# Kernel tuning notes

Hardware: AMD Instinct MI355X
Metric: run time of the kernel (lower is better)

The kernel has to match this reference:

```python
import jax, jax.numpy as jnp
import numpy as np

B = 16384      # batch
H = 512        # experts_hidden
E = 5          # num_experts
T = 2          # num_tasks
OUT = 128      # fixed protein expert output width (from .view(-1, E, 1, 128))


def setup_inputs() -> dict:
    key = jax.random.key(0)
    ks = jax.random.split(key, 12)
    s = 0.02  # init scale
    return {
        "share_x": jax.random.normal(ks[0], (B, H), jnp.float32),
        "task_x0": jax.random.normal(ks[1], (B, H), jnp.float32),
        "task_x1": jax.random.normal(ks[2], (B, H), jnp.float32),
        # shared experts: stacked weights for all E experts
        "share_W1": jax.random.normal(ks[3], (E, H, H), jnp.float32) * s,
        "share_b1": jnp.zeros((E, H), jnp.float32),
        "share_W2": jax.random.normal(ks[4], (E, H, OUT), jnp.float32) * s,
        "share_b2": jnp.zeros((E, OUT), jnp.float32),
        # task experts: [T, E, ...]
        "task_W1": jax.random.normal(ks[5], (T, E, H, H), jnp.float32) * s,
        "task_b1": jnp.zeros((T, E, H), jnp.float32),
        "task_W2": jax.random.normal(ks[6], (T, E, H, OUT), jnp.float32) * s,
        "task_b2": jnp.zeros((T, E, OUT), jnp.float32),
    }


def _expert_bank(x, W1, b1, W2, b2):
    """Run all E experts on x in one batched GEMM pair.

    x: [B, H]; W1: [E, H, H]; W2: [E, H, OUT].
    Equivalent to torch.concat([e(x) for e in experts], dim=0)
    followed by .view(-1, E, 1, OUT).
    """
    h = jax.nn.relu(jnp.einsum('bh,ehk->ebk', x, W1) + b1[:, None, :])  # [E,B,H]
    o = jnp.einsum('ebk,eko->ebo', h, W2) + b2[:, None, :]              # [E,B,OUT]
    # concat along dim 0 == flatten (E,B) -> E*B, then view(-1, E, 1, OUT)
    return o.reshape(-1, E, 1, OUT)


def reference(share_x, task_x0, task_x1,
              share_W1, share_b1, share_W2, share_b2,
              task_W1, task_b1, task_W2, task_b2):
    share_out = _expert_bank(share_x, share_W1, share_b1, share_W2, share_b2)
    task_xs = (task_x0, task_x1)
    task_outs = tuple(
        _expert_bank(task_xs[i], task_W1[i], task_b1[i], task_W2[i], task_b2[i])
        for i in range(T)
    )
    return (share_out,) + task_outs
```

## Files before the change

kernel.cpp:

```cpp
#include <hip/hip_runtime.h>

#define H 512
#define OW 128
#define NB 16384

typedef float f32x4 __attribute__((ext_vector_type(4)));
typedef short short8 __attribute__((ext_vector_type(8)));
typedef unsigned short ushort8v __attribute__((ext_vector_type(8)));

static __device__ __forceinline__ unsigned short f2bf(float f) {
    union { float f; unsigned u; } v; v.f = f;
    return (unsigned short)((v.u + 0x7FFFu + ((v.u >> 16) & 1u)) >> 16);
}

static __device__ __forceinline__ f32x4 mfma16(short8 a, short8 b, f32x4 c) {
    return __builtin_amdgcn_mfma_f32_16x16x32_bf16(a, b, c, 0, 0, 0);
}

static __device__ __forceinline__ void gll16(const unsigned short* g, unsigned short* l) {
    __builtin_amdgcn_global_load_lds(
        (__attribute__((address_space(1))) void*)g,
        (__attribute__((address_space(3))) void*)l, 16, 0, 0);
}

static __device__ __forceinline__ short8 sw_read(const unsigned short* l, int row, int ch) {
    return *(const short8*)&l[row * 64 + ((ch ^ (row & 7)) << 3)];
}

__global__ void prep_w1(const float* __restrict__ share_W1,
                        const float* __restrict__ task_W1,
                        unsigned short* __restrict__ w1t) {
    const int inst = blockIdx.z;
    const float* src = (inst < 5) ? (share_W1 + (size_t)inst * H * H)
                                  : (task_W1 + (size_t)(inst - 5) * H * H);
    unsigned short* dst = w1t + (size_t)inst * H * H;
    const int g = blockIdx.x * 256 + threadIdx.x;
    const int n = g & (H - 1);
    const int kc = g >> 9;
    float v[8];
#pragma unroll
    for (int i = 0; i < 8; ++i) v[i] = src[(size_t)(kc * 8 + i) * H + n];
    ushort8v o;
#pragma unroll
    for (int i = 0; i < 8; ++i) o[i] = f2bf(v[i]);
    *(ushort8v*)&dst[(size_t)n * H + kc * 8] = o;
}

__global__ void prep_w2(const float* __restrict__ share_W2,
                        const float* __restrict__ task_W2,
                        unsigned short* __restrict__ w2t) {
    const int inst = blockIdx.z;
    const float* src = (inst < 5) ? (share_W2 + (size_t)inst * H * OW)
                                  : (task_W2 + (size_t)(inst - 5) * H * OW);
    unsigned short* dst = w2t + (size_t)inst * OW * H;
    const int g = blockIdx.x * 256 + threadIdx.x;
    const int n = g & (OW - 1);
    const int kc = g >> 7;
    float v[8];
#pragma unroll
    for (int i = 0; i < 8; ++i) v[i] = src[(size_t)(kc * 8 + i) * OW + n];
    ushort8v o;
#pragma unroll
    for (int i = 0; i < 8; ++i) o[i] = f2bf(v[i]);
    *(ushort8v*)&dst[(size_t)n * H + kc * 8] = o;
}

__global__ void prep_x(const float* __restrict__ x0, const float* __restrict__ x1,
                       const float* __restrict__ x2, unsigned short* __restrict__ xb) {
    const int z = blockIdx.z;
    const float* s = (z == 0) ? x0 : (z == 1 ? x1 : x2);
    const size_t g = (size_t)(blockIdx.x * 256 + threadIdx.x) * 8;
    float4 a = *(const float4*)&s[g];
    float4 b = *(const float4*)&s[g + 4];
    ushort8v o;
    o[0] = f2bf(a.x); o[1] = f2bf(a.y); o[2] = f2bf(a.z); o[3] = f2bf(a.w);
    o[4] = f2bf(b.x); o[5] = f2bf(b.y); o[6] = f2bf(b.z); o[7] = f2bf(b.w);
    *(ushort8v*)&xb[(size_t)z * NB * H + g] = o;
}

__global__ __launch_bounds__(256, 2) void fused(
    const unsigned short* __restrict__ xb, const unsigned short* __restrict__ w1t,
    const unsigned short* __restrict__ w2t,
    const float* __restrict__ share_b1, const float* __restrict__ task_b1,
    const float* __restrict__ share_b2, const float* __restrict__ task_b2,
    float* __restrict__ out)
{
    __shared__ unsigned short smem[33792];
    unsigned short* sA  = smem;
    unsigned short* sB  = smem + 8192;
    unsigned short* sH  = smem + 16384;
    unsigned short* sW0 = smem;
    unsigned short* sW1 = smem + 8192;

    const int tid = threadIdx.x;
    const int lane = tid & 63;
    const int wave = tid >> 6;
    const int wy = wave >> 1, wx = wave & 1;
    const int lm = lane & 15, lq = lane >> 4;
    const int prow = lane >> 3;
    const int lch  = (lane & 7) ^ prow;

    const int swz = (blockIdx.x & 7) * 240 + (blockIdx.x >> 3);
    const int z = swz / 640;
    const int rzi = swz % 640;
    const int rowtile = rzi / 5;
    const int e = rzi % 5;
    const int inst = z * 5 + e;

    const unsigned short* xp  = xb + ((size_t)z * NB + rowtile * 128) * H;
    const unsigned short* w1p = w1t + (size_t)inst * H * H;
    const unsigned short* w2p = w2t + (size_t)inst * OW * H;
    const float* b1 = (z == 0) ? (share_b1 + e * H) : (task_b1 + ((z - 1) * 5 + e) * H);
    const float* b2 = (z == 0) ? (share_b2 + e * OW) : (task_b2 + ((z - 1) * 5 + e) * OW);
    float* op = out + ((size_t)inst * NB + rowtile * 128) * OW;

    const f32x4 zero4 = {0.f, 0.f, 0.f, 0.f};
    f32x4 acc2[4][4];
#pragma unroll
    for (int i = 0; i < 4; ++i)
#pragma unroll
        for (int j = 0; j < 4; ++j) acc2[i][j] = zero4;

    for (int nt = 0; nt < 4; ++nt) {
        const unsigned short* wnp = w1p + (size_t)(nt * 128) * H;

        f32x4 acc1[4][4];
#pragma unroll
        for (int i = 0; i < 4; ++i)
#pragma unroll
            for (int j = 0; j < 4; ++j) acc1[i][j] = zero4;

        for (int kt = 0; kt < 8; ++kt) {
            __syncthreads();
#pragma unroll
            for (int t = 0; t < 4; ++t) {
                const int row = wave * 32 + t * 8 + prow;
                const int lo = wave * 2048 + t * 512;
                gll16(&xp [(size_t)row * H + kt * 64 + lch * 8], &sA[lo]);
                gll16(&wnp[(size_t)row * H + kt * 64 + lch * 8], &sB[lo]);
            }
            __syncthreads();
#pragma unroll
            for (int kk = 0; kk < 2; ++kk) {
                short8 af[4], bfr[4];
#pragma unroll
                for (int i = 0; i < 4; ++i) af[i] = sw_read(sA, wy * 64 + i * 16 + lm, kk * 4 + lq);
#pragma unroll
                for (int j = 0; j < 4; ++j) bfr[j] = sw_read(sB, wx * 64 + j * 16 + lm, kk * 4 + lq);
#pragma unroll
                for (int i = 0; i < 4; ++i)
#pragma unroll
                    for (int j = 0; j < 4; ++j) acc1[i][j] = mfma16(af[i], bfr[j], acc1[i][j]);
            }
        }
        __syncthreads();

#pragma unroll
        for (int t = 0; t < 4; ++t) {
            const int row = wave * 32 + t * 8 + prow;
            const int lo = wave * 2048 + t * 512;
            gll16(&w2p[(size_t)row * H + nt * 128 +      lch * 8], &sW0[lo]);
            gll16(&w2p[(size_t)row * H + nt * 128 + 64 + lch * 8], &sW1[lo]);
        }

#pragma unroll
        for (int j = 0; j < 4; ++j) {
            const int col = wx * 64 + j * 16 + lm;
            const float b1v = b1[nt * 128 + col];
#pragma unroll
            for (int i = 0; i < 4; ++i)
#pragma unroll
                for (int rr = 0; rr < 4; ++rr) {
                    const int row = wy * 64 + i * 16 + lq * 4 + rr;
                    sH[row * 136 + col] = f2bf(fmaxf(acc1[i][j][rr] + b1v, 0.f));
                }
        }
        __syncthreads();

#pragma unroll
        for (int kk = 0; kk < 4; ++kk) {
            short8 af[4], bfr[4];
#pragma unroll
            for (int i = 0; i < 4; ++i)
                af[i] = *(const short8*)&sH[(wy * 64 + i * 16 + lm) * 136 + kk * 32 + lq * 8];
#pragma unroll
            for (int j = 0; j < 4; ++j)
                bfr[j] = sw_read((kk & 2) ? sW1 : sW0, wx * 64 + j * 16 + lm, (kk & 1) * 4 + lq);
#pragma unroll
            for (int i = 0; i < 4; ++i)
#pragma unroll
                for (int j = 0; j < 4; ++j) acc2[i][j] = mfma16(af[i], bfr[j], acc2[i][j]);
        }
    }

#pragma unroll
    for (int j = 0; j < 4; ++j) {
        const int col = wx * 64 + j * 16 + lm;
        const float b2v = b2[col];
#pragma unroll
        for (int i = 0; i < 4; ++i)
#pragma unroll
            for (int rr = 0; rr < 4; ++rr) {
                const int row = wy * 64 + i * 16 + lq * 4 + rr;
                op[(size_t)row * OW + col] = acc2[i][j][rr] + b2v;
            }
    }
}

extern "C" void kernel_launch(void* const* d_in, const int* in_sizes, int n_in,
                              void* d_out, int out_size, void* d_ws, size_t ws_size,
                              hipStream_t stream) {
    const float* share_x  = (const float*)d_in[0];
    const float* task_x0  = (const float*)d_in[1];
    const float* task_x1  = (const float*)d_in[2];
    const float* share_W1 = (const float*)d_in[3];
    const float* share_b1 = (const float*)d_in[4];
    const float* share_W2 = (const float*)d_in[5];
    const float* share_b2 = (const float*)d_in[6];
    const float* task_W1  = (const float*)d_in[7];
    const float* task_b1  = (const float*)d_in[8];
    const float* task_W2  = (const float*)d_in[9];
    const float* task_b2  = (const float*)d_in[10];
    float* out = (float*)d_out;

    unsigned short* w1t = (unsigned short*)d_ws;
    unsigned short* w2t = w1t + (size_t)15 * H * H;
    unsigned short* xb  = w2t + (size_t)15 * OW * H;

    prep_w1<<<dim3(128, 1, 15), 256, 0, stream>>>(share_W1, task_W1, w1t);
    prep_w2<<<dim3(32, 1, 15), 256, 0, stream>>>(share_W2, task_W2, w2t);
    prep_x <<<dim3(4096, 1, 3), 256, 0, stream>>>(share_x, task_x0, task_x1, xb);
    fused<<<1920, 256, 0, stream>>>(xb, w1t, w2t, share_b1, task_b1,
                                    share_b2, task_b2, out);
}
```

Before: 414.4 us.

## Double-buffer GEMM1 K-loop with async LDS loads and register-resident W2 fragments

Restructures the first GEMM's K loop into a double-buffered pipeline with 32-wide K steps. The next stage's global-to-LDS loads are issued while the current stage computes, using explicit vmcnt waits and raw s_barrier instead of full __syncthreads. W2 is pre-permuted on the host-side prep kernel into MFMA fragment order, so each wave loads its B fragments straight into registers rather than staging them through LDS. MFMA sections are also wrapped in s_setprio. This adds register pressure (16 short8 for W2), relies on hand-counted vmcnt values being correct, and the next tile's first stages are prefetched across the nt boundary.

```diff
diff --git a/kernel.cpp b/kernel.cpp
--- a/kernel.cpp
+++ b/kernel.cpp
@@ -23,9 +23,9 @@
         (__attribute__((address_space(3))) void*)l, 16, 0, 0);
 }
 
-static __device__ __forceinline__ short8 sw_read(const unsigned short* l, int row, int ch) {
-    return *(const short8*)&l[row * 64 + ((ch ^ (row & 7)) << 3)];
-}
+#define WAITB(n) asm volatile("s_waitcnt vmcnt(" #n ")\n\ts_barrier" ::: "memory")
+#define RELB()   asm volatile("s_barrier" ::: "memory")
+#define CFENCE() asm volatile("" ::: "memory")
 
 __global__ void prep_w1(const float* __restrict__ share_W1,
                         const float* __restrict__ task_W1,
@@ -48,21 +48,26 @@
 
 __global__ void prep_w2(const float* __restrict__ share_W2,
                         const float* __restrict__ task_W2,
-                        unsigned short* __restrict__ w2t) {
+                        unsigned short* __restrict__ w2f) {
     const int inst = blockIdx.z;
     const float* src = (inst < 5) ? (share_W2 + (size_t)inst * H * OW)
                                   : (task_W2 + (size_t)(inst - 5) * H * OW);
-    unsigned short* dst = w2t + (size_t)inst * OW * H;
+    unsigned short* dst = w2f + (size_t)inst * H * OW;
     const int g = blockIdx.x * 256 + threadIdx.x;
-    const int n = g & (OW - 1);
-    const int kc = g >> 7;
+    const int l  = g & 63;
+    const int f  = (g >> 6) & 15;
+    const int kk = f >> 2, j = f & 3;
+    const int wx = (g >> 10) & 1;
+    const int nt = (g >> 11) & 3;
+    const int n  = wx * 64 + j * 16 + (l & 15);
+    const int k0 = nt * 128 + kk * 32 + ((l >> 4) & 3) * 8;
     float v[8];
 #pragma unroll
-    for (int i = 0; i < 8; ++i) v[i] = src[(size_t)(kc * 8 + i) * OW + n];
+    for (int i = 0; i < 8; ++i) v[i] = src[(size_t)(k0 + i) * OW + n];
     ushort8v o;
 #pragma unroll
     for (int i = 0; i < 8; ++i) o[i] = f2bf(v[i]);
-    *(ushort8v*)&dst[(size_t)n * H + kc * 8] = o;
+    *(ushort8v*)&dst[(size_t)g * 8] = o;
 }
 
 __global__ void prep_x(const float* __restrict__ x0, const float* __restrict__ x1,
@@ -80,25 +85,22 @@
 
 __global__ __launch_bounds__(256, 2) void fused(
     const unsigned short* __restrict__ xb, const unsigned short* __restrict__ w1t,
-    const unsigned short* __restrict__ w2t,
+    const unsigned short* __restrict__ w2f,
     const float* __restrict__ share_b1, const float* __restrict__ task_b1,
     const float* __restrict__ share_b2, const float* __restrict__ task_b2,
     float* __restrict__ out)
 {
     __shared__ unsigned short smem[33792];
-    unsigned short* sA  = smem;
-    unsigned short* sB  = smem + 8192;
-    unsigned short* sH  = smem + 16384;
-    unsigned short* sW0 = smem;
-    unsigned short* sW1 = smem + 8192;
+    unsigned short* sH = smem + 16384;
 
     const int tid = threadIdx.x;
     const int lane = tid & 63;
     const int wave = tid >> 6;
     const int wy = wave >> 1, wx = wave & 1;
     const int lm = lane & 15, lq = lane >> 4;
-    const int prow = lane >> 3;
-    const int lch  = (lane & 7) ^ prow;
+    const int r4 = lane >> 2;
+    const int c4 = lane & 3;
+    const int sc4 = c4 ^ (r4 & 3);
 
     const int swz = (blockIdx.x & 7) * 240 + (blockIdx.x >> 3);
     const int z = swz / 640;
@@ -109,7 +111,7 @@
 
     const unsigned short* xp  = xb + ((size_t)z * NB + rowtile * 128) * H;
     const unsigned short* w1p = w1t + (size_t)inst * H * H;
-    const unsigned short* w2p = w2t + (size_t)inst * OW * H;
+    const unsigned short* w2b = w2f + (size_t)inst * H * OW + (size_t)lane * 8;
     const float* b1 = (z == 0) ? (share_b1 + e * H) : (task_b1 + ((z - 1) * 5 + e) * H);
     const float* b2 = (z == 0) ? (share_b2 + e * OW) : (task_b2 + ((z - 1) * 5 + e) * OW);
     float* op = out + ((size_t)inst * NB + rowtile * 128) * OW;
@@ -121,47 +123,67 @@
 #pragma unroll
         for (int j = 0; j < 4; ++j) acc2[i][j] = zero4;
 
+    f32x4 acc1[4][4];
+
+    auto STAGE = [&](int kt, int buf, const unsigned short* wsrc) {
+        unsigned short* a = smem + buf * 4096;
+        unsigned short* b = smem + 8192 + buf * 4096;
+        const int ko = kt * 32 + sc4 * 8;
+#pragma unroll
+        for (int t = 0; t < 2; ++t) {
+            gll16(&xp  [(size_t)(wave * 32 + t * 16 + r4) * H + ko], &a[wave * 1024 + t * 512]);
+            gll16(&wsrc[(size_t)(wave * 32 + t * 16 + r4) * H + ko], &b[wave * 1024 + t * 512]);
+        }
+    };
+
+    auto COMPUTE = [&](int buf) {
+        const unsigned short* a = smem + buf * 4096;
+        const unsigned short* b = smem + 8192 + buf * 4096;
+        const int sw = (lq ^ (lm & 3)) << 3;
+        short8 af[4], bq[4];
+#pragma unroll
+        for (int i = 0; i < 4; ++i) af[i] = *(const short8*)&a[(wy * 64 + i * 16 + lm) * 32 + sw];
+#pragma unroll
+        for (int j = 0; j < 4; ++j) bq[j] = *(const short8*)&b[(wx * 64 + j * 16 + lm) * 32 + sw];
+        __builtin_amdgcn_s_setprio(1);
+#pragma unroll
+        for (int i = 0; i < 4; ++i)
+#pragma unroll
+            for (int j = 0; j < 4; ++j) acc1[i][j] = mfma16(af[i], bq[j], acc1[i][j]);
+        __builtin_amdgcn_s_setprio(0);
+    };
+
+    STAGE(0, 0, w1p);
+    STAGE(1, 1, w1p);
+
     for (int nt = 0; nt < 4; ++nt) {
         const unsigned short* wnp = w1p + (size_t)(nt * 128) * H;
-
-        f32x4 acc1[4][4];
+        const unsigned short* wnx = w1p + (size_t)(((nt + 1) & 3) * 128) * H;
+
+        CFENCE();
+        short8 rW2[16];
+        {
+            const unsigned short* wb = w2b + (size_t)(nt * 2 + wx) * 16 * 512;
+#pragma unroll
+            for (int f = 0; f < 16; ++f) rW2[f] = *(const short8*)&wb[f * 512];
+        }
+        CFENCE();
+
 #pragma unroll
         for (int i = 0; i < 4; ++i)
 #pragma unroll
             for (int j = 0; j < 4; ++j) acc1[i][j] = zero4;
 
-        for (int kt = 0; kt < 8; ++kt) {
-            __syncthreads();
-#pragma unroll
-            for (int t = 0; t < 4; ++t) {
-                const int row = wave * 32 + t * 8 + prow;
-                const int lo = wave * 2048 + t * 512;
-                gll16(&xp [(size_t)row * H + kt * 64 + lch * 8], &sA[lo]);
-                gll16(&wnp[(size_t)row * H + kt * 64 + lch * 8], &sB[lo]);
-            }
-            __syncthreads();
-#pragma unroll
-            for (int kk = 0; kk < 2; ++kk) {
-                short8 af[4], bfr[4];
-#pragma unroll
-                for (int i = 0; i < 4; ++i) af[i] = sw_read(sA, wy * 64 + i * 16 + lm, kk * 4 + lq);
-#pragma unroll
-                for (int j = 0; j < 4; ++j) bfr[j] = sw_read(sB, wx * 64 + j * 16 + lm, kk * 4 + lq);
-#pragma unroll
-                for (int i = 0; i < 4; ++i)
-#pragma unroll
-                    for (int j = 0; j < 4; ++j) acc1[i][j] = mfma16(af[i], bfr[j], acc1[i][j]);
-            }
-        }
-        __syncthreads();
-
-#pragma unroll
-        for (int t = 0; t < 4; ++t) {
-            const int row = wave * 32 + t * 8 + prow;
-            const int lo = wave * 2048 + t * 512;
-            gll16(&w2p[(size_t)row * H + nt * 128 +      lch * 8], &sW0[lo]);
-            gll16(&w2p[(size_t)row * H + nt * 128 + 64 + lch * 8], &sW1[lo]);
-        }
+        WAITB(20); COMPUTE(0); RELB(); STAGE(2, 0, wnp);
+        WAITB(20); COMPUTE(1); RELB(); STAGE(3, 1, wnp);
+        for (int kt = 2; kt < 14; ++kt) {
+            WAITB(4); COMPUTE(kt & 1); RELB(); STAGE(kt + 2, kt & 1, wnp);
+        }
+        WAITB(4); COMPUTE(0); RELB();
+        if (nt < 3) STAGE(0, 0, wnx);
+        if (nt < 3) { WAITB(4); } else { WAITB(0); }
+        COMPUTE(1); RELB();
+        if (nt < 3) STAGE(1, 1, wnx);
 
 #pragma unroll
         for (int j = 0; j < 4; ++j) {
@@ -175,21 +197,20 @@
                     sH[row * 136 + col] = f2bf(fmaxf(acc1[i][j][rr] + b1v, 0.f));
                 }
         }
-        __syncthreads();
+        asm volatile("s_waitcnt lgkmcnt(0)\n\ts_barrier" ::: "memory");
 
 #pragma unroll
         for (int kk = 0; kk < 4; ++kk) {
-            short8 af[4], bfr[4];
+            short8 ah[4];
 #pragma unroll
             for (int i = 0; i < 4; ++i)
-                af[i] = *(const short8*)&sH[(wy * 64 + i * 16 + lm) * 136 + kk * 32 + lq * 8];
-#pragma unroll
-            for (int j = 0; j < 4; ++j)
-                bfr[j] = sw_read((kk & 2) ? sW1 : sW0, wx * 64 + j * 16 + lm, (kk & 1) * 4 + lq);
+                ah[i] = *(const short8*)&sH[(wy * 64 + i * 16 + lm) * 136 + kk * 32 + lq * 8];
+            __builtin_amdgcn_s_setprio(1);
 #pragma unroll
             for (int i = 0; i < 4; ++i)
 #pragma unroll
-                for (int j = 0; j < 4; ++j) acc2[i][j] = mfma16(af[i], bfr[j], acc2[i][j]);
+                for (int j = 0; j < 4; ++j) acc2[i][j] = mfma16(ah[i], rW2[kk * 4 + j], acc2[i][j]);
+            __builtin_amdgcn_s_setprio(0);
         }
     }
 
@@ -224,12 +245,12 @@
     float* out = (float*)d_out;
 
     unsigned short* w1t = (unsigned short*)d_ws;
-    unsigned short* w2t = w1t + (size_t)15 * H * H;
-    unsigned short* xb  = w2t + (size_t)15 * OW * H;
+    unsigned short* w2f = w1t + (size_t)15 * H * H;
+    unsigned short* xb  = w2f + (size_t)15 * OW * H;
 
     prep_w1<<<dim3(128, 1, 15), 256, 0, stream>>>(share_W1, task_W1, w1t);
-    prep_w2<<<dim3(32, 1, 15), 256, 0, stream>>>(share_W2, task_W2, w2t);
+    prep_w2<<<dim3(32, 1, 15), 256, 0, stream>>>(share_W2, task_W2, w2f);
     prep_x <<<dim3(4096, 1, 3), 256, 0, stream>>>(share_x, task_x0, task_x1, xb);
-    fused<<<1920, 256, 0, stream>>>(xb, w1t, w2t, share_b1, task_b1,
+    fused<<<1920, 256, 0, stream>>>(xb, w1t, w2f, share_b1, task_b1,
                                     share_b2, task_b2, out);
 }
```

Measured after the change: 596.7 us. 44.0% more time.
